# Optimization experiments

Measured on AMD Instinct MI355X. Metric: run time of the kernel, lower is better.

The kernel has to match this reference:

```python
import jax, jax.numpy as jnp
import numpy as np

D_MODEL = 1024
NUM_HEADS = 16
D_K = D_MODEL // NUM_HEADS
B, L = 2, 2048
NEG = -1e9


def setup_inputs() -> dict:
    key = jax.random.key(0)
    ks = jax.random.split(key, 11)
    s = 1.0 / np.sqrt(D_MODEL)
    inp = {
        "Q": jax.random.normal(ks[0], (B, L, D_MODEL), jnp.float32),
        "K": jax.random.normal(ks[1], (B, L, D_MODEL), jnp.float32),
        "V": jax.random.normal(ks[2], (B, L, D_MODEL), jnp.float32),
        # causal mask: True = valid (attend), False = masked
        "mask": jnp.tril(jnp.ones((L, L), bool))[None, None],
        # torch nn.Linear weights stored [out, in]
        "Wq": jax.random.normal(ks[3], (D_MODEL, D_MODEL), jnp.float32) * s,
        "bq": jnp.zeros((D_MODEL,), jnp.float32),
        "Wk": jax.random.normal(ks[4], (D_MODEL, D_MODEL), jnp.float32) * s,
        "bk": jnp.zeros((D_MODEL,), jnp.float32),
        "Wv": jax.random.normal(ks[5], (D_MODEL, D_MODEL), jnp.float32) * s,
        "bv": jnp.zeros((D_MODEL,), jnp.float32),
        "Wo": jax.random.normal(ks[6], (D_MODEL, D_MODEL), jnp.float32) * s,
        "bo": jnp.zeros((D_MODEL,), jnp.float32),
    }
    return inp


def _split_heads(x):  # [B,L,D] -> [B,H,L,d_k]
    b, l, _ = x.shape
    return x.reshape(b, l, NUM_HEADS, D_K).transpose(0, 2, 1, 3)


def reference(Q, K, V, mask, Wq, bq, Wk, bk, Wv, bv, Wo, bo):
    # linear projections (torch Linear: x @ W.T + b)
    q = _split_heads(Q @ Wq.T + bq)
    k = _split_heads(K @ Wk.T + bk)
    v = _split_heads(V @ Wv.T + bv)
    scores = jnp.einsum("bhqd,bhkd->bhqk", q, k) / jnp.sqrt(jnp.float32(D_K))
    scores = jnp.where(mask, scores, NEG)
    probs = jax.nn.softmax(scores, axis=-1)  # dropout inactive at inference
    attn = jnp.einsum("bhqk,bhkd->bhqd", probs, v)
    b, h, l, dk = attn.shape
    o_in = attn.transpose(0, 2, 1, 3).reshape(b, l, D_MODEL)
    return o_in @ Wo.T + bo
```

## Files before the change

### kernel.cpp

```cpp
#include <hip/hip_runtime.h>
#include <stdint.h>

#define D_MODEL 1024
#define NH 16
#define DK 64
#define BBATCH 2
#define LL 2048
#define SCALE_LOG2E 0.1803368801111244f

typedef unsigned short bfu;
typedef __attribute__((ext_vector_type(8))) short bf16x8;
typedef __attribute__((ext_vector_type(4))) float f32x4;

union BF8 { uint32_t w[4]; bf16x8 v; };

__device__ __forceinline__ bfu f2bf(float f) {
    union { float f; uint32_t u; } a; a.f = f;
    uint32_t r = a.u + 0x7FFF + ((a.u >> 16) & 1);
    return (bfu)(r >> 16);
}
__device__ __forceinline__ uint32_t pktrunc(float hi, float lo) {
    return __builtin_amdgcn_perm(__float_as_uint(hi), __float_as_uint(lo), 0x07060302);
}

__device__ __forceinline__ void gload_lds16(const void* g, void* l) {
    __builtin_amdgcn_global_load_lds(
        (const __attribute__((address_space(1))) void*)g,
        (__attribute__((address_space(3))) void*)l, 16, 0, 0);
}

__device__ __forceinline__ int swz(int R, int G) {
    return R * 64 + (((G ^ (R & 7))) << 3);
}

__device__ __forceinline__ uint4 ld8_f32_to_bf16(const float* g, float sc) {
    const float4* s = (const float4*)g;
    float4 u = s[0], v = s[1];
    u.x *= sc; u.y *= sc; u.z *= sc; u.w *= sc;
    v.x *= sc; v.y *= sc; v.z *= sc; v.w *= sc;
    uint4 w;
    w.x = pktrunc(u.y, u.x); w.y = pktrunc(u.w, u.z);
    w.z = pktrunc(v.y, v.x); w.w = pktrunc(v.w, v.z);
    return w;
}

#define BM 128
#define BN 128
#define BKK 64

__device__ __forceinline__ int kperm(int k) {
    return (((k >> 4) & 1) << 5) | (((k >> 2) & 3) << 3) | (((k >> 5) & 1) << 2) | (k & 3);
}

__global__ __launch_bounds__(256, 2) void gemm_proj(
    const float* __restrict__ Qf, const float* __restrict__ Kf, const float* __restrict__ Vf,
    const float* __restrict__ Wqf, const float* __restrict__ Wkf, const float* __restrict__ Wvf,
    const float* __restrict__ bq, const float* __restrict__ bk, const float* __restrict__ bv,
    bfu* __restrict__ qp, bfu* __restrict__ kp, bfu* __restrict__ vt)
{
    const int id = blockIdx.x;
    const int xcd = id & 7, q = id >> 3;
    const int zy = xcd * 12 + (q >> 3);
    const int x  = q & 7;
    const int z  = zy >> 5, y = zy & 31;

    const float* A = (z == 0) ? Qf : ((z == 1) ? Kf : Vf);
    const float* B = (z == 0) ? Wqf : ((z == 1) ? Wkf : Wvf);
    const float* bias = (z == 0) ? bq : ((z == 1) ? bk : bv);
    const float bsc = (z == 0) ? SCALE_LOG2E : 1.0f;
    bfu* out = (z == 0) ? qp : ((z == 1) ? kp : vt);

    __shared__ __align__(16) bfu As[BM * BKK];
    __shared__ __align__(16) bfu Bs[BN * BKK];

    const int t = threadIdx.x;
    const int lane = t & 63;
    const int wave = t >> 6;
    const int wm = wave & 1, wn = wave >> 1;
    const int tm = y * BM, tn = x * BN;
    const int lr = lane & 15, quad = lane >> 4;

    f32x4 acc[4][4];
    for (int i = 0; i < 4; i++) for (int j = 0; j < 4; j++) acc[i][j] = (f32x4){0.f, 0.f, 0.f, 0.f};

    for (int kt = 0; kt < 1024; kt += BKK) {
        for (int it = 0; it < 4; ++it) {
            int c = t + it * 256;
            int row = c >> 3, gx = (c & 7) ^ (row & 7);
            uint4 w = ld8_f32_to_bf16(&A[(size_t)(tm + row) * 1024 + kt + gx * 8], 1.0f);
            *(uint4*)&As[(size_t)c * 8] = w;
        }
        for (int it = 0; it < 4; ++it) {
            int c = t + it * 256;
            int row = c >> 3, gx = (c & 7) ^ (row & 7);
            uint4 w = ld8_f32_to_bf16(&B[(size_t)(tn + row) * 1024 + kt + gx * 8], bsc);
            *(uint4*)&Bs[(size_t)c * 8] = w;
        }
        __syncthreads();
        for (int kx = 0; kx < 2; kx++) {
            bf16x8 a[4], b[4];
            for (int i = 0; i < 4; i++)
                a[i] = *(const bf16x8*)&As[swz(wm * 64 + i * 16 + lr, kx * 4 + quad)];
            for (int i = 0; i < 4; i++)
                b[i] = *(const bf16x8*)&Bs[swz(wn * 64 + i * 16 + lr, kx * 4 + quad)];
            for (int mt = 0; mt < 4; mt++)
                for (int nt = 0; nt < 4; nt++)
                    acc[mt][nt] = __builtin_amdgcn_mfma_f32_16x16x32_bf16(a[mt], b[nt], acc[mt][nt], 0, 0, 0);
        }
        __syncthreads();
    }

    for (int mt = 0; mt < 4; mt++)
        for (int nt = 0; nt < 4; nt++)
            for (int r = 0; r < 4; r++) {
                int m = tm + wm * 64 + mt * 16 + quad * 4 + r;
                int n = tn + wn * 64 + nt * 16 + lr;
                float v = acc[mt][nt][r] + bias[n] * bsc;
                int b_ = m >> 11, l = m & 2047;
                int h = n >> 6, d = n & 63;
                if (z < 2)
                    out[((size_t)((b_ * NH + h) * LL + l)) * DK + d] = f2bf(v);
                else {
                    int lp = (l & ~63) | kperm(l & 63);
                    out[((size_t)((b_ * NH + h) * DK + d)) * LL + lp] = f2bf(v);
                }
            }
}

__global__ __launch_bounds__(256, 2) void attn_kernel(
    const bfu* __restrict__ qp, const bfu* __restrict__ kp, const bfu* __restrict__ vtp,
    bfu* __restrict__ attn)
{
    const int id = blockIdx.x;
    const int bh = (id & 7) | (((id >> 3) & 3) << 3);
    const int band = 31 - (id >> 5);
    const int b_ = bh >> 4, h = bh & 15;
    const int t = threadIdx.x;
    const int lane = t & 63, w = t >> 6;
    const int hw = w & 1;
    const int jh = w >> 1;
    const int lr = lane & 15, quad = lane >> 4, q8 = quad << 3;

    __shared__ __align__(16) bfu Ks[2][2][64 * 64];
    __shared__ __align__(16) bfu Vs[2][2][64 * 64];

    const int n  = band + 1;
    const int n0 = (n + 1) >> 1;
    const int nj = (jh == 0) ? n0 : (n - n0);
    const int jb = (jh == 0) ? 0 : n0;

    const int tl = t & 127;
    const int r0 = band * 64 + hw * 32;

    const bfu* kbase = kp + (size_t)bh * LL * DK;
    const bfu* vbase = vtp + (size_t)bh * DK * LL;

    bf16x8 aq[2][2];
    for (int mt = 0; mt < 2; mt++)
        for (int kx = 0; kx < 2; kx++)
            aq[mt][kx] = *(const bf16x8*)&qp[((size_t)bh * LL + r0 + mt * 16 + lr) * DK + kx * 32 + q8];

    f32x4 o[2][4];
    for (int mt = 0; mt < 2; mt++)
        for (int nf = 0; nf < 4; nf++) o[mt][nf] = (f32x4){0.f, 0.f, 0.f, 0.f};
    float lsum[2] = {0.f, 0.f};

    if (nj > 0) {
        for (int it = 0; it < 4; ++it) {
            int c = tl + it * 128;
            int r = c >> 3, gx = (c & 7) ^ (r & 7);
            gload_lds16(&kbase[(size_t)(jb * 64 + r) * DK + gx * 8], &Ks[jh][0][(size_t)c * 8]);
            gload_lds16(&vbase[(size_t)r * LL + jb * 64 + gx * 8], &Vs[jh][0][(size_t)c * 8]);
        }
    }
    __syncthreads();

    for (int i = 0; i < n0; ++i) {
        const int buf = i & 1;
        if (i + 1 < nj) {
            const int nb = buf ^ 1, jn = jb + i + 1;
            for (int it = 0; it < 4; ++it) {
                int c = tl + it * 128;
                int r = c >> 3, gx = (c & 7) ^ (r & 7);
                gload_lds16(&kbase[(size_t)(jn * 64 + r) * DK + gx * 8], &Ks[jh][nb][(size_t)c * 8]);
                gload_lds16(&vbase[(size_t)r * LL + jn * 64 + gx * 8], &Vs[jh][nb][(size_t)c * 8]);
            }
        }
        if (i < nj) {
            const int j = jb + i;
            const bfu* Kt = Ks[jh][buf];
            const bfu* Vt = Vs[jh][buf];
            f32x4 sv[4][2];
            for (int kt = 0; kt < 4; kt++)
                for (int mt = 0; mt < 2; mt++) sv[kt][mt] = (f32x4){0.f, 0.f, 0.f, 0.f};
            for (int kx = 0; kx < 2; kx++)
                for (int kt = 0; kt < 4; kt++) {
                    bf16x8 ak = *(const bf16x8*)&Kt[swz(kt * 16 + lr, kx * 4 + quad)];
                    for (int mt = 0; mt < 2; mt++)
                        sv[kt][mt] = __builtin_amdgcn_mfma_f32_16x16x32_bf16(ak, aq[mt][kx], sv[kt][mt], 0, 0, 0);
                }
            if (j == band) {
                const int mb = r0 & 63;
                for (int kt = 0; kt < 4; kt++)
                    for (int mt = 0; mt < 2; mt++)
                        for (int r = 0; r < 4; r++) {
                            int kl = kt * 16 + quad * 4 + r;
                            int ml = mb + mt * 16 + lr;
                            if (kl > ml) sv[kt][mt][r] = -1e9f;
                        }
            }
            for (int kt = 0; kt < 4; kt++)
                for (int mt = 0; mt < 2; mt++)
                    for (int r = 0; r < 4; r++) {
                        float e = __builtin_amdgcn_exp2f(sv[kt][mt][r]);
                        sv[kt][mt][r] = e;
                        lsum[mt] += e;
                    }
            for (int kx = 0; kx < 2; kx++) {
                BF8 pf[2];
                for (int mt = 0; mt < 2; mt++) {
                    pf[mt].w[0] = pktrunc(sv[kx][mt][1], sv[kx][mt][0]);
                    pf[mt].w[1] = pktrunc(sv[kx][mt][3], sv[kx][mt][2]);
                    pf[mt].w[2] = pktrunc(sv[2 + kx][mt][1], sv[2 + kx][mt][0]);
                    pf[mt].w[3] = pktrunc(sv[2 + kx][mt][3], sv[2 + kx][mt][2]);
                }
                for (int nf = 0; nf < 4; nf++) {
                    bf16x8 av = *(const bf16x8*)&Vt[swz(nf * 16 + lr, kx * 4 + quad)];
                    for (int mt = 0; mt < 2; mt++)
                        o[mt][nf] = __builtin_amdgcn_mfma_f32_16x16x32_bf16(av, pf[mt].v, o[mt][nf], 0, 0, 0);
                }
            }
        }
        __syncthreads();
    }

    float* Of = (float*)&Ks[0][0][0];
    float* Lf = (float*)&Vs[0][0][0];
    const int ci = hw * 64 + lane;
    if (jh == 1) {
        float* dst = Of + ci * 33;
        for (int mt = 0; mt < 2; mt++)
            for (int nf = 0; nf < 4; nf++)
                for (int r = 0; r < 4; r++)
                    dst[mt * 16 + nf * 4 + r] = o[mt][nf][r];
        Lf[ci * 2 + 0] = lsum[0];
        Lf[ci * 2 + 1] = lsum[1];
    }
    __syncthreads();
    if (jh == 0) {
        const float* src = Of + ci * 33;
        for (int mt = 0; mt < 2; mt++)
            for (int nf = 0; nf < 4; nf++)
                for (int r = 0; r < 4; r++)
                    o[mt][nf][r] += src[mt * 16 + nf * 4 + r];
        lsum[0] += Lf[ci * 2 + 0];
        lsum[1] += Lf[ci * 2 + 1];

        for (int mt = 0; mt < 2; mt++) {
            float l = lsum[mt];
            l += __shfl_xor(l, 16);
            l += __shfl_xor(l, 32);
            float rinv = 1.0f / l;
            for (int nf = 0; nf < 4; nf++) {
                uint32_t w0 = ((uint32_t)f2bf(o[mt][nf][1] * rinv) << 16) | f2bf(o[mt][nf][0] * rinv);
                uint32_t w1 = ((uint32_t)f2bf(o[mt][nf][3] * rinv) << 16) | f2bf(o[mt][nf][2] * rinv);
                uint2 pk2 = {w0, w1};
                *(uint2*)&attn[((size_t)(b_ * LL + r0 + mt * 16 + lr)) * D_MODEL + h * DK + nf * 16 + quad * 4] = pk2;
            }
        }
    }
}

#define OBM 128
#define OBN 64

__global__ __launch_bounds__(256) void gemm_out(
    const bfu* __restrict__ A, const float* __restrict__ B,
    const float* __restrict__ bias, float* __restrict__ out)
{
    __shared__ __align__(16) bfu As[OBM * 64];
    __shared__ __align__(16) bfu Bs[OBN * 64];

    const int t = threadIdx.x;
    const int lane = t & 63, w = t >> 6;
    const int tm = blockIdx.y * OBM, tn = blockIdx.x * OBN;
    const int lr = lane & 15, quad = lane >> 4;

    f32x4 acc[2][4];
    for (int i = 0; i < 2; i++) for (int j = 0; j < 4; j++) acc[i][j] = (f32x4){0.f, 0.f, 0.f, 0.f};

    for (int kt = 0; kt < 1024; kt += 64) {
        for (int it = 0; it < 4; ++it) {
            int c = t + it * 256;
            int row = c >> 3, gx = (c & 7) ^ (row & 7);
            gload_lds16(&A[(size_t)(tm + row) * 1024 + kt + gx * 8], &As[(size_t)c * 8]);
        }
        for (int it = 0; it < 2; ++it) {
            int c = t + it * 256;
            int row = c >> 3, gx = (c & 7) ^ (row & 7);
            uint4 wv = ld8_f32_to_bf16(&B[(size_t)(tn + row) * 1024 + kt + gx * 8], 1.0f);
            *(uint4*)&Bs[(size_t)c * 8] = wv;
        }
        __syncthreads();
        for (int kx = 0; kx < 2; kx++) {
            bf16x8 a[2], b[4];
            for (int mt = 0; mt < 2; mt++)
                a[mt] = *(const bf16x8*)&As[swz(w * 32 + mt * 16 + lr, kx * 4 + quad)];
            for (int nt = 0; nt < 4; nt++)
                b[nt] = *(const bf16x8*)&Bs[swz(nt * 16 + lr, kx * 4 + quad)];
            for (int mt = 0; mt < 2; mt++)
                for (int nt = 0; nt < 4; nt++)
                    acc[mt][nt] = __builtin_amdgcn_mfma_f32_16x16x32_bf16(a[mt], b[nt], acc[mt][nt], 0, 0, 0);
        }
        __syncthreads();
    }

    for (int mt = 0; mt < 2; mt++)
        for (int nt = 0; nt < 4; nt++)
            for (int r = 0; r < 4; r++) {
                int m = tm + w * 32 + mt * 16 + quad * 4 + r;
                int n = tn + nt * 16 + lr;
                out[(size_t)m * D_MODEL + n] = acc[mt][nt][r] + bias[n];
            }
}

extern "C" void kernel_launch(void* const* d_in, const int* in_sizes, int n_in,
                              void* d_out, int out_size, void* d_ws, size_t ws_size,
                              hipStream_t stream) {
    const float* Q  = (const float*)d_in[0];
    const float* K  = (const float*)d_in[1];
    const float* V  = (const float*)d_in[2];
    const float* Wq = (const float*)d_in[4];
    const float* bq = (const float*)d_in[5];
    const float* Wk = (const float*)d_in[6];
    const float* bk = (const float*)d_in[7];
    const float* Wv = (const float*)d_in[8];
    const float* bv = (const float*)d_in[9];
    const float* Wo = (const float*)d_in[10];
    const float* bo = (const float*)d_in[11];
    float* out = (float*)d_out;

    char* ws = (char*)d_ws;
    bfu* qp  = (bfu*)(ws + ((size_t)0  << 20));
    bfu* kp  = (bfu*)(ws + ((size_t)8  << 20));
    bfu* vt  = (bfu*)(ws + ((size_t)16 << 20));
    bfu* attn = (bfu*)(ws + ((size_t)24 << 20));

    gemm_proj<<<768, 256, 0, stream>>>(Q, K, V, Wq, Wk, Wv,
                                       bq, bk, bv, qp, kp, vt);

    attn_kernel<<<dim3(1024), 256, 0, stream>>>(qp, kp, vt, attn);

    gemm_out<<<dim3(16, 32), 256, 0, stream>>>(attn, Wo, bo, out);
}
```

Before: 267.0 us.

## Register-prefetch next K tile of fp32 operands in projection and output GEMMs

Both GEMM kernels now load the next K-slice of fp32 inputs into registers while the current slice is converted and consumed from LDS, hiding global load latency behind MFMA work. The trailing barrier moves to the top of the loop. gemm_out also gets a launch-bounds hint of 2 blocks per CU. The prefetch buffers raise register pressure, which could cut occupancy or cause spills in gemm_proj.

New measurement: 232.9 us. 1.15x faster.

```diff
diff --git a/kernel.cpp b/kernel.cpp
--- a/kernel.cpp
+++ b/kernel.cpp
@@ -22,26 +22,23 @@
 __device__ __forceinline__ uint32_t pktrunc(float hi, float lo) {
     return __builtin_amdgcn_perm(__float_as_uint(hi), __float_as_uint(lo), 0x07060302);
 }
-
-__device__ __forceinline__ void gload_lds16(const void* g, void* l) {
-    __builtin_amdgcn_global_load_lds(
-        (const __attribute__((address_space(1))) void*)g,
-        (__attribute__((address_space(3))) void*)l, 16, 0, 0);
-}
-
-__device__ __forceinline__ int swz(int R, int G) {
-    return R * 64 + (((G ^ (R & 7))) << 3);
-}
-
-__device__ __forceinline__ uint4 ld8_f32_to_bf16(const float* g, float sc) {
-    const float4* s = (const float4*)g;
-    float4 u = s[0], v = s[1];
+__device__ __forceinline__ uint4 pack8(float4 u, float4 v, float sc) {
     u.x *= sc; u.y *= sc; u.z *= sc; u.w *= sc;
     v.x *= sc; v.y *= sc; v.z *= sc; v.w *= sc;
     uint4 w;
     w.x = pktrunc(u.y, u.x); w.y = pktrunc(u.w, u.z);
     w.z = pktrunc(v.y, v.x); w.w = pktrunc(v.w, v.z);
     return w;
+}
+
+__device__ __forceinline__ void gload_lds16(const void* g, void* l) {
+    __builtin_amdgcn_global_load_lds(
+        (const __attribute__((address_space(1))) void*)g,
+        (__attribute__((address_space(3))) void*)l, 16, 0, 0);
+}
+
+__device__ __forceinline__ int swz(int R, int G) {
+    return R * 64 + (((G ^ (R & 7))) << 3);
 }
 
 #define BM 128
@@ -80,21 +77,38 @@
     const int tm = y * BM, tn = x * BN;
     const int lr = lane & 15, quad = lane >> 4;
 
+    int arow[4], acol[4];
+    for (int it = 0; it < 4; ++it) {
+        int c = t + it * 256;
+        arow[it] = c >> 3;
+        acol[it] = ((c & 7) ^ ((c >> 3) & 7)) * 8;
+    }
+
     f32x4 acc[4][4];
     for (int i = 0; i < 4; i++) for (int j = 0; j < 4; j++) acc[i][j] = (f32x4){0.f, 0.f, 0.f, 0.f};
 
+    float4 ra[4][2], rb[4][2];
+    for (int it = 0; it < 4; ++it) {
+        const float4* pa = (const float4*)&A[(size_t)(tm + arow[it]) * 1024 + 0 + acol[it]];
+        ra[it][0] = pa[0]; ra[it][1] = pa[1];
+        const float4* pb = (const float4*)&B[(size_t)(tn + arow[it]) * 1024 + 0 + acol[it]];
+        rb[it][0] = pb[0]; rb[it][1] = pb[1];
+    }
+
     for (int kt = 0; kt < 1024; kt += BKK) {
+        if (kt) __syncthreads();
         for (int it = 0; it < 4; ++it) {
             int c = t + it * 256;
-            int row = c >> 3, gx = (c & 7) ^ (row & 7);
-            uint4 w = ld8_f32_to_bf16(&A[(size_t)(tm + row) * 1024 + kt + gx * 8], 1.0f);
-            *(uint4*)&As[(size_t)c * 8] = w;
-        }
-        for (int it = 0; it < 4; ++it) {
-            int c = t + it * 256;
-            int row = c >> 3, gx = (c & 7) ^ (row & 7);
-            uint4 w = ld8_f32_to_bf16(&B[(size_t)(tn + row) * 1024 + kt + gx * 8], bsc);
-            *(uint4*)&Bs[(size_t)c * 8] = w;
+            *(uint4*)&As[(size_t)c * 8] = pack8(ra[it][0], ra[it][1], 1.0f);
+            *(uint4*)&Bs[(size_t)c * 8] = pack8(rb[it][0], rb[it][1], bsc);
+        }
+        if (kt + BKK < 1024) {
+            for (int it = 0; it < 4; ++it) {
+                const float4* pa = (const float4*)&A[(size_t)(tm + arow[it]) * 1024 + kt + BKK + acol[it]];
+                ra[it][0] = pa[0]; ra[it][1] = pa[1];
+                const float4* pb = (const float4*)&B[(size_t)(tn + arow[it]) * 1024 + kt + BKK + acol[it]];
+                rb[it][0] = pb[0]; rb[it][1] = pb[1];
+            }
         }
         __syncthreads();
         for (int kx = 0; kx < 2; kx++) {
@@ -107,7 +121,6 @@
                 for (int nt = 0; nt < 4; nt++)
                     acc[mt][nt] = __builtin_amdgcn_mfma_f32_16x16x32_bf16(a[mt], b[nt], acc[mt][nt], 0, 0, 0);
         }
-        __syncthreads();
     }
 
     for (int mt = 0; mt < 4; mt++)
@@ -274,7 +287,7 @@
 #define OBM 128
 #define OBN 64
 
-__global__ __launch_bounds__(256) void gemm_out(
+__global__ __launch_bounds__(256, 2) void gemm_out(
     const bfu* __restrict__ A, const float* __restrict__ B,
     const float* __restrict__ bias, float* __restrict__ out)
 {
@@ -286,20 +299,36 @@
     const int tm = blockIdx.y * OBM, tn = blockIdx.x * OBN;
     const int lr = lane & 15, quad = lane >> 4;
 
+    int brow[2], bcol[2];
+    for (int it = 0; it < 2; ++it) {
+        int c = t + it * 256;
+        brow[it] = c >> 3;
+        bcol[it] = ((c & 7) ^ ((c >> 3) & 7)) * 8;
+    }
+
     f32x4 acc[2][4];
     for (int i = 0; i < 2; i++) for (int j = 0; j < 4; j++) acc[i][j] = (f32x4){0.f, 0.f, 0.f, 0.f};
 
+    float4 rb[2][2];
+    for (int it = 0; it < 2; ++it) {
+        const float4* pb = (const float4*)&B[(size_t)(tn + brow[it]) * 1024 + 0 + bcol[it]];
+        rb[it][0] = pb[0]; rb[it][1] = pb[1];
+    }
+
     for (int kt = 0; kt < 1024; kt += 64) {
+        if (kt) __syncthreads();
+        for (int it = 0; it < 2; ++it)
+            *(uint4*)&Bs[(size_t)(t + it * 256) * 8] = pack8(rb[it][0], rb[it][1], 1.0f);
         for (int it = 0; it < 4; ++it) {
             int c = t + it * 256;
             int row = c >> 3, gx = (c & 7) ^ (row & 7);
             gload_lds16(&A[(size_t)(tm + row) * 1024 + kt + gx * 8], &As[(size_t)c * 8]);
         }
-        for (int it = 0; it < 2; ++it) {
-            int c = t + it * 256;
-            int row = c >> 3, gx = (c & 7) ^ (row & 7);
-            uint4 wv = ld8_f32_to_bf16(&B[(size_t)(tn + row) * 1024 + kt + gx * 8], 1.0f);
-            *(uint4*)&Bs[(size_t)c * 8] = wv;
+        if (kt + 64 < 1024) {
+            for (int it = 0; it < 2; ++it) {
+                const float4* pb = (const float4*)&B[(size_t)(tn + brow[it]) * 1024 + kt + 64 + bcol[it]];
+                rb[it][0] = pb[0]; rb[it][1] = pb[1];
+            }
         }
         __syncthreads();
         for (int kx = 0; kx < 2; kx++) {
@@ -312,7 +341,6 @@
                 for (int nt = 0; nt < 4; nt++)
                     acc[mt][nt] = __builtin_amdgcn_mfma_f32_16x16x32_bf16(a[mt], b[nt], acc[mt][nt], 0, 0, 0);
         }
-        __syncthreads();
     }
 
     for (int mt = 0; mt < 2; mt++)
```
